# Performance work log

Hardware: AMD Instinct MI355X
Metric: run time of the kernel (lower is better)

The kernel has to match this reference:

```python
import jax, jax.numpy as jnp
import numpy as np

EMBED_DIM = 1024
NUM_HEADS = 16
HEAD_DIM = EMBED_DIM // NUM_HEADS
B, S = 2, 2048


def setup_inputs() -> dict:
    key = jax.random.key(0)
    k = jax.random.split(key, 8)
    scale = 1.0 / np.sqrt(EMBED_DIM)
    return {
        "x": jax.random.normal(k[0], (B, S, EMBED_DIM), dtype=jnp.float32),
        "x1": jax.random.normal(k[1], (B, S, EMBED_DIM), dtype=jnp.float32),
        "x2": jax.random.normal(k[2], (B, S, EMBED_DIM), dtype=jnp.float32),
        "qkv_w": jax.random.normal(k[3], (3 * EMBED_DIM, EMBED_DIM), dtype=jnp.float32) * scale,
        "qkv_b": jnp.zeros((3 * EMBED_DIM,), dtype=jnp.float32),
        "out_w": jax.random.normal(k[4], (EMBED_DIM, EMBED_DIM), dtype=jnp.float32) * scale,
        "out_b": jnp.zeros((EMBED_DIM,), dtype=jnp.float32),
    }


def reference(x, x1, x2, qkv_w, qkv_b, out_w, out_b):
    # x1, x2 are accepted but unused, matching the torch module.
    b, s, e = x.shape
    qkv = x @ qkv_w.T + qkv_b                      # [B,S,3E]
    qkv = qkv.reshape(b, s, 3, NUM_HEADS, HEAD_DIM)
    qkv = jnp.transpose(qkv, (2, 0, 3, 1, 4))      # [3,B,H,S,D]
    q, k, v = qkv[0], qkv[1], qkv[2]
    scores = jnp.einsum("bhqd,bhkd->bhqk", q, k) / np.sqrt(HEAD_DIM)
    probs = jax.nn.sigmoid(scores)                 # [B,H,S,S]
    sample = jax.random.bernoulli(jax.random.key(42), probs).astype(probs.dtype)
    # straight-through: forward uses sample, gradient flows as identity to probs
    attn = probs + jax.lax.stop_gradient(sample - probs)
    out = jnp.einsum("bhqk,bhkd->bhqd", attn, v)   # [B,H,S,D]
    out = jnp.transpose(out, (0, 2, 1, 3)).reshape(b, s, e)
    return out @ out_w.T + out_b
```

## Files before the change

### kernel.cpp

```cpp
#include <hip/hip_runtime.h>
#include <stdint.h>

#define NB 2
#define NS 2048
#define NE 1024
#define NH 16
#define ND 64

typedef __attribute__((ext_vector_type(8))) short short8;
typedef __attribute__((ext_vector_type(4))) float f4;
typedef __attribute__((ext_vector_type(4))) unsigned short us4;

static __device__ __forceinline__ unsigned short bf16_rne(float x) {
  uint32_t u = __builtin_bit_cast(uint32_t, x);
  u += 0x7fffu + ((u >> 16) & 1u);
  return (unsigned short)(u >> 16);
}
static __device__ __forceinline__ float bf16_f32(unsigned short h) {
  uint32_t u = ((uint32_t)h) << 16;
  return __builtin_bit_cast(float, u);
}

static __device__ __forceinline__ void threefry42(uint32_t x0, uint32_t x1,
                                                  uint32_t& o0, uint32_t& o1) {
  const uint32_t ks0 = 0u, ks1 = 42u;
  const uint32_t ks2 = 0u ^ 42u ^ 0x1BD11BDAu;
  x0 += ks0; x1 += ks1;
#define TF4(a,b,c,d) \
  x0 += x1; x1 = __builtin_rotateleft32(x1, a); x1 ^= x0; \
  x0 += x1; x1 = __builtin_rotateleft32(x1, b); x1 ^= x0; \
  x0 += x1; x1 = __builtin_rotateleft32(x1, c); x1 ^= x0; \
  x0 += x1; x1 = __builtin_rotateleft32(x1, d); x1 ^= x0;
  TF4(13,15,26,6)  x0 += ks1; x1 += ks2 + 1u;
  TF4(17,29,16,24) x0 += ks2; x1 += ks0 + 2u;
  TF4(13,15,26,6)  x0 += ks0; x1 += ks1 + 3u;
  TF4(17,29,16,24) x0 += ks1; x1 += ks2 + 4u;
  TF4(13,15,26,6)  x0 += ks2; x1 += ks0 + 5u;
#undef TF4
  o0 = x0; o1 = x1;
}

static __device__ __forceinline__ void gl2lds16(const void* g, void* l) {
  __builtin_amdgcn_global_load_lds(
      (const __attribute__((address_space(1))) uint32_t*)g,
      (__attribute__((address_space(3))) uint32_t*)l, 16, 0, 0);
}

__global__ void k_split(const float* __restrict__ x, const float* __restrict__ qw,
                        const float* __restrict__ ow,
                        unsigned short* __restrict__ xh, unsigned short* __restrict__ xl,
                        unsigned short* __restrict__ wh, unsigned short* __restrict__ wl,
                        unsigned short* __restrict__ woh) {
  for (uint32_t i = blockIdx.x * 256u + threadIdx.x; i < 8388608u; i += gridDim.x * 256u) {
    if (i < 4194304u) {
      float v = x[i];
      unsigned short hi = bf16_rne(v);
      xh[i] = hi;
      xl[i] = bf16_rne(v - bf16_f32(hi));
    } else if (i < 7340032u) {
      uint32_t j = i - 4194304u;
      float v = qw[j];
      unsigned short hi = bf16_rne(v);
      wh[j] = hi;
      wl[j] = bf16_rne(v - bf16_f32(hi));
    } else {
      uint32_t j = i - 7340032u;
      woh[j] = bf16_rne(ow[j]);
    }
  }
}

__global__ __launch_bounds__(256) void k_qkv(
    const unsigned short* __restrict__ xh, const unsigned short* __restrict__ xl,
    const unsigned short* __restrict__ wh, const unsigned short* __restrict__ wl,
    const float* __restrict__ qkv_b,
    unsigned short* __restrict__ Qh, unsigned short* __restrict__ Ql,
    unsigned short* __restrict__ Kh, unsigned short* __restrict__ Kl,
    unsigned short* __restrict__ Vt) {
  __shared__ unsigned short SM[16384];
  unsigned short* Ah = SM;
  unsigned short* Al = SM + 4096;
  unsigned short* Bh = SM + 8192;
  unsigned short* Bl = SM + 12288;
  const int tid = threadIdx.x;
  const int lane = tid & 63, wid = tid >> 6;
  const int wm = wid >> 1, wn = wid & 1;
  const int bn = blockIdx.x, bm = blockIdx.y;
  const bool isV = (bn >= 16);
  const int quad = lane >> 4, c16 = lane & 15;
  const int ldrow = lane >> 2;
  const int ldk = (lane & 3) * 8;

  f4 acc[4][4];
#pragma unroll
  for (int a = 0; a < 4; ++a)
#pragma unroll
    for (int b = 0; b < 4; ++b) { f4 z = {0.f, 0.f, 0.f, 0.f}; acc[a][b] = z; }

  for (int kt = 0; kt < 32; ++kt) {
    const int k0 = kt * 32;
    __syncthreads();
#pragma unroll
    for (int r = 0; r < 2; ++r) {
      const int c = wid + r * 4;
      const int grow = c * 16 + ldrow;
      const size_t ao = (size_t)(bm * 128 + grow) * 1024 + k0 + ldk;
      const size_t bo = (size_t)(bn * 128 + grow) * 1024 + k0 + ldk;
      const int lo = c * 512 + lane * 8;
      gl2lds16(xh + ao, &Ah[lo]);
      gl2lds16(wh + bo, &Bh[lo]);
      if (!isV) {
        gl2lds16(xl + ao, &Al[lo]);
        gl2lds16(wl + bo, &Bl[lo]);
      }
    }
    __syncthreads();

    short8 ah[4], al[4], bhf[4], blf[4];
#pragma unroll
    for (int t = 0; t < 4; ++t) {
      ah[t] = *(const short8*)&Ah[(wm * 64 + t * 16 + c16) * 32 + quad * 8];
      bhf[t] = *(const short8*)&Bh[(wn * 64 + t * 16 + c16) * 32 + quad * 8];
      if (!isV) {
        al[t] = *(const short8*)&Al[(wm * 64 + t * 16 + c16) * 32 + quad * 8];
        blf[t] = *(const short8*)&Bl[(wn * 64 + t * 16 + c16) * 32 + quad * 8];
      }
    }
    if (isV) {
#pragma unroll
      for (int tm = 0; tm < 4; ++tm)
#pragma unroll
        for (int tn = 0; tn < 4; ++tn)
          acc[tm][tn] = __builtin_amdgcn_mfma_f32_16x16x32_bf16(ah[tm], bhf[tn], acc[tm][tn], 0, 0, 0);
    } else {
#pragma unroll
      for (int tm = 0; tm < 4; ++tm)
#pragma unroll
        for (int tn = 0; tn < 4; ++tn) {
          acc[tm][tn] = __builtin_amdgcn_mfma_f32_16x16x32_bf16(ah[tm], bhf[tn], acc[tm][tn], 0, 0, 0);
          acc[tm][tn] = __builtin_amdgcn_mfma_f32_16x16x32_bf16(ah[tm], blf[tn], acc[tm][tn], 0, 0, 0);
          acc[tm][tn] = __builtin_amdgcn_mfma_f32_16x16x32_bf16(al[tm], bhf[tn], acc[tm][tn], 0, 0, 0);
        }
    }
  }

  if (!isV) {
#pragma unroll
    for (int tm = 0; tm < 4; ++tm) {
#pragma unroll
      for (int tn = 0; tn < 4; ++tn) {
        const int j = bn * 128 + wn * 64 + tn * 16 + c16;
        const float bias = qkv_b[j];
        const int which = j >> 10;
        const int rem = j & 1023;
        const int h = rem >> 6, d = rem & 63;
#pragma unroll
        for (int r = 0; r < 4; ++r) {
          const int i = bm * 128 + wm * 64 + tm * 16 + quad * 4 + r;
          const int b = i >> 11, s = i & 2047;
          const size_t off = (((size_t)(b * 16 + h)) * 2048 + (size_t)s) * 64 + d;
          const float v = acc[tm][tn][r] + bias;
          const unsigned short hi = bf16_rne(v);
          const unsigned short lo = bf16_rne(v - bf16_f32(hi));
          if (which == 0) { Qh[off] = hi; Ql[off] = lo; }
          else            { Kh[off] = hi; Kl[off] = lo; }
        }
      }
    }
  } else {
    __syncthreads();
#pragma unroll
    for (int tm = 0; tm < 4; ++tm) {
#pragma unroll
      for (int tn = 0; tn < 4; ++tn) {
        const int j = bn * 128 + wn * 64 + tn * 16 + c16;
        const float bias = qkv_b[j];
        const int d_local = wn * 64 + tn * 16 + c16;
#pragma unroll
        for (int r = 0; r < 4; ++r) {
          const int s_local = wm * 64 + tm * 16 + quad * 4 + r;
          SM[d_local * 128 + s_local] = bf16_rne(acc[tm][tn][r] + bias);
        }
      }
    }
    __syncthreads();
    const int b = (bm * 128) >> 11;
    const int s0 = (bm * 128) & 2047;
    const int h2 = (bn - 16) * 2;
#pragma unroll
    for (int it = 0; it < 8; ++it) {
      const int chunk = it * 256 + tid;
      const int dr = chunk >> 4;
      const int sc = (chunk & 15) * 8;
      const short8 v = *(const short8*)&SM[dr * 128 + sc];
      const int bh = b * 16 + h2 + (dr >> 6);
      const int d = dr & 63;
      *(short8*)&Vt[((size_t)bh * 64 + d) * 2048 + s0 + sc] = v;
    }
  }
}

__global__ __launch_bounds__(512, 8) void k_attn(
    const unsigned short* __restrict__ Qh, const unsigned short* __restrict__ Ql,
    const unsigned short* __restrict__ Khg, const unsigned short* __restrict__ Klg,
    const unsigned short* __restrict__ Vtg, unsigned short* __restrict__ AO) {
  __shared__ unsigned short Ksh[4096], Ksl[4096], Vs[8192];
  __shared__ unsigned char Pmb[8192];
  const int tid = threadIdx.x;
  const int lane = tid & 63, w = tid >> 6;
  const int quad = lane >> 4, c16 = lane & 15;
  const int q0 = blockIdx.x * 128;
  const int bh = blockIdx.y;
  const int ks = blockIdx.z;
  const int kbase = ks * 1024;
  const size_t base = (size_t)bh * (size_t)(2048 * 64);
  unsigned short* AOp = AO + (size_t)ks * 4194304u;

  const size_t qoff = base + (size_t)(q0 + w * 16 + c16) * 64 + quad * 8;
  const short8 qh0 = *(const short8*)&Qh[qoff];
  const short8 qh1 = *(const short8*)&Qh[qoff + 32];
  const short8 ql0 = *(const short8*)&Ql[qoff];
  const short8 ql1 = *(const short8*)&Ql[qoff + 32];

  const uint32_t fb = (uint32_t)bh * 4194304u +
                      (uint32_t)(q0 + w * 16 + quad * 4) * 2048u + (uint32_t)c16;

  const int r0 = tid >> 3, g0 = ((tid & 7) - r0) & 7;

  f4 oacc[4];
#pragma unroll
  for (int s = 0; s < 4; ++s) { f4 z = {0.f, 0.f, 0.f, 0.f}; oacc[s] = z; }

  auto stage = [&](int kb, int vbuf) {
    const size_t koff = base + (size_t)kb * 64;
    gl2lds16(Khg + koff + r0 * 64 + g0 * 8, &Ksh[tid * 8]);
    gl2lds16(Klg + koff + r0 * 64 + g0 * 8, &Ksl[tid * 8]);
    gl2lds16(Vtg + base + (size_t)r0 * 2048 + kb + g0 * 8, &Vs[vbuf * 4096 + tid * 8]);
  };

  stage(kbase, 0);

  for (int kt = 0; kt < 16; ++kt) {
    const int kb = kbase + kt * 64;
    const int vb = (kt & 1) * 4096;
    __syncthreads();

    f4 sacc[4];
#pragma unroll
    for (int sub = 0; sub < 4; ++sub) {
      const int rK = sub * 16 + c16;
      const int sA = ((quad + rK) & 7) * 8;
      const int sB = ((quad + 4 + rK) & 7) * 8;
      const short8 kh0 = *(const short8*)&Ksh[rK * 64 + sA];
      const short8 kh1 = *(const short8*)&Ksh[rK * 64 + sB];
      const short8 kl0 = *(const short8*)&Ksl[rK * 64 + sA];
      const short8 kl1 = *(const short8*)&Ksl[rK * 64 + sB];
      f4 s = {0.f, 0.f, 0.f, 0.f};
      s = __builtin_amdgcn_mfma_f32_16x16x32_bf16(qh0, kh0, s, 0, 0, 0);
      s = __builtin_amdgcn_mfma_f32_16x16x32_bf16(qh1, kh1, s, 0, 0, 0);
      s = __builtin_amdgcn_mfma_f32_16x16x32_bf16(qh0, kl0, s, 0, 0, 0);
      s = __builtin_amdgcn_mfma_f32_16x16x32_bf16(qh1, kl1, s, 0, 0, 0);
      s = __builtin_amdgcn_mfma_f32_16x16x32_bf16(ql0, kh0, s, 0, 0, 0);
      s = __builtin_amdgcn_mfma_f32_16x16x32_bf16(ql1, kh1, s, 0, 0, 0);
      sacc[sub] = s;
    }
    __syncthreads();
    if (kt < 15) stage(kb + 64, (kt & 1) ^ 1);

#pragma unroll
    for (int sub = 0; sub < 4; ++sub) {
#pragma unroll
      for (int rr = 0; rr < 4; ++rr) {
        const uint32_t f = fb + (uint32_t)(rr * 2048) + (uint32_t)(kb + sub * 16);
        uint32_t o0, o1;
        threefry42(0u, f, o0, o1);
        const float m = (float)((o0 ^ o1) >> 9);
        const float e = __builtin_amdgcn_exp2f(sacc[sub][rr] * -0.18033688f);
        const int row = w * 16 + quad * 4 + rr;
        Pmb[row * 64 + sub * 16 + c16] = (fmaf(m, e, m) < 8388608.0f) ? 0x40u : 0u;
      }
    }

    const int rp = w * 16 + c16;
    const uint32_t plo0 = *(const uint32_t*)&Pmb[rp * 64 + quad * 8];
    const uint32_t phi0 = *(const uint32_t*)&Pmb[rp * 64 + quad * 8 + 4];
    const uint32_t plo1 = *(const uint32_t*)&Pmb[rp * 64 + 32 + quad * 8];
    const uint32_t phi1 = *(const uint32_t*)&Pmb[rp * 64 + 32 + quad * 8 + 4];
    short8 pa0, pa1;
#pragma unroll
    for (int j = 0; j < 4; ++j) {
      pa0[j]     = (plo0 & (0x40u << (8 * j))) ? (short)0x3F80 : (short)0;
      pa0[j + 4] = (phi0 & (0x40u << (8 * j))) ? (short)0x3F80 : (short)0;
      pa1[j]     = (plo1 & (0x40u << (8 * j))) ? (short)0x3F80 : (short)0;
      pa1[j + 4] = (phi1 & (0x40u << (8 * j))) ? (short)0x3F80 : (short)0;
    }
#pragma unroll
    for (int sub = 0; sub < 4; ++sub) {
      const int rV = sub * 16 + c16;
      const short8 vv0 = *(const short8*)&Vs[vb + rV * 64 + ((quad + rV) & 7) * 8];
      const short8 vv1 = *(const short8*)&Vs[vb + rV * 64 + ((quad + 4 + rV) & 7) * 8];
      oacc[sub] = __builtin_amdgcn_mfma_f32_16x16x32_bf16(pa0, vv0, oacc[sub], 0, 0, 0);
      oacc[sub] = __builtin_amdgcn_mfma_f32_16x16x32_bf16(pa1, vv1, oacc[sub], 0, 0, 0);
    }
  }

  const int b = bh >> 4, hh = bh & 15;
#pragma unroll
  for (int sub = 0; sub < 4; ++sub)
#pragma unroll
    for (int r = 0; r < 4; ++r) {
      const int srow = b * 2048 + q0 + w * 16 + quad * 4 + r;
      AOp[(size_t)srow * 1024 + hh * 64 + sub * 16 + c16] = bf16_rne(oacc[sub][r]);
    }
}

__global__ __launch_bounds__(256) void k_out(
    const unsigned short* __restrict__ A0, const unsigned short* __restrict__ A1,
    const unsigned short* __restrict__ Bw,
    const float* __restrict__ out_b, float* __restrict__ out) {
  __shared__ unsigned short As[128 * 32], Bs[128 * 32];
  const int tid = threadIdx.x;
  const int lane = tid & 63, wid = tid >> 6;
  const int wm = wid >> 1, wn = wid & 1;
  const int bn = blockIdx.x, bm = blockIdx.y;
  const int quad = lane >> 4, c16 = lane & 15;
  const int ldrow = lane >> 2;
  const int ldk = (lane & 3) * 8;

  f4 acc[4][4];
#pragma unroll
  for (int a = 0; a < 4; ++a)
#pragma unroll
    for (int b = 0; b < 4; ++b) { f4 z = {0.f, 0.f, 0.f, 0.f}; acc[a][b] = z; }

  for (int kt = 0; kt < 32; ++kt) {
    const int k0 = kt * 32;
    __syncthreads();
#pragma unroll
    for (int r = 0; r < 2; ++r) {
      const int c = wid + r * 4;
      const int grow = c * 16 + ldrow;
      const size_t ao = (size_t)(bm * 128 + grow) * 1024 + k0 + ldk;
      const size_t bo = (size_t)(bn * 128 + grow) * 1024 + k0 + ldk;
      const int lo = c * 512 + lane * 8;
      const short8 a0 = *(const short8*)&A0[ao];
      const short8 a1 = *(const short8*)&A1[ao];
      short8 acm;
#pragma unroll
      for (int j = 0; j < 8; ++j)
        acm[j] = (short)bf16_rne(bf16_f32((unsigned short)a0[j]) +
                                 bf16_f32((unsigned short)a1[j]));
      *(short8*)&As[lo] = acm;
      gl2lds16(Bw + bo, &Bs[lo]);
    }
    __syncthreads();

    short8 af[4], bf[4];
#pragma unroll
    for (int t = 0; t < 4; ++t) {
      af[t] = *(const short8*)&As[(wm * 64 + t * 16 + c16) * 32 + quad * 8];
      bf[t] = *(const short8*)&Bs[(wn * 64 + t * 16 + c16) * 32 + quad * 8];
    }
#pragma unroll
    for (int tm = 0; tm < 4; ++tm)
#pragma unroll
      for (int tn = 0; tn < 4; ++tn)
        acc[tm][tn] = __builtin_amdgcn_mfma_f32_16x16x32_bf16(af[tm], bf[tn], acc[tm][tn], 0, 0, 0);
  }

#pragma unroll
  for (int tm = 0; tm < 4; ++tm) {
#pragma unroll
    for (int tn = 0; tn < 4; ++tn) {
      const int j = bn * 128 + wn * 64 + tn * 16 + c16;
      const float bias = out_b[j];
#pragma unroll
      for (int r = 0; r < 4; ++r) {
        const int i = bm * 128 + wm * 64 + tm * 16 + quad * 4 + r;
        out[(size_t)i * 1024 + j] = acc[tm][tn][r] + bias;
      }
    }
  }
}

extern "C" void kernel_launch(void* const* d_in, const int* in_sizes, int n_in,
                              void* d_out, int out_size, void* d_ws, size_t ws_size,
                              hipStream_t stream) {
  const float* x     = (const float*)d_in[0];
  const float* qkv_w = (const float*)d_in[3];
  const float* qkv_b = (const float*)d_in[4];
  const float* out_w = (const float*)d_in[5];
  const float* out_b = (const float*)d_in[6];
  float* out = (float*)d_out;

  unsigned short* xh  = (unsigned short*)d_ws;
  unsigned short* xl  = xh + 4194304;
  unsigned short* wh  = xl + 4194304;
  unsigned short* wl  = wh + 3145728;
  unsigned short* woh = wl + 3145728;
  unsigned short* Vt  = woh + 1048576;
  unsigned short* Qh  = Vt + 4194304;
  unsigned short* Ql  = Qh + 4194304;
  unsigned short* Kh  = Ql + 4194304;
  unsigned short* Kl  = Kh + 4194304;
  unsigned short* AO0 = xh;
  unsigned short* AO1 = xl;

  k_split<<<8192, 256, 0, stream>>>(x, qkv_w, out_w, xh, xl, wh, wl, woh);
  k_qkv<<<dim3(24, 32), 256, 0, stream>>>(xh, xl, wh, wl, qkv_b, Qh, Ql, Kh, Kl, Vt);
  k_attn<<<dim3(16, 32, 2), 512, 0, stream>>>(Qh, Ql, Kh, Kl, Vt, AO0);
  k_out<<<dim3(8, 32), 256, 0, stream>>>(AO0, AO1, woh, out_b, out);
}
```

Baseline: 562.1 us.

## Shrink attention blocks to 64 queries and transpose masks via ds_bpermute

The attention kernel now uses 256-thread blocks covering 64 query rows, with twice as many blocks, and each thread stages two chunks of K/V per tile. The shared-memory byte mask used to transpose the Bernoulli sample from MFMA output layout to A-operand layout is replaced by per-lane bitmasks exchanged through ds_bpermute. This removes the LDS mask buffer and its writes and reads. In exchange, each K/V tile is loaded from global memory twice as often in total, and the lane shuffles add instructions.

```diff
diff --git a/kernel.cpp b/kernel.cpp
--- a/kernel.cpp
+++ b/kernel.cpp
@@ -200,16 +200,15 @@
   }
 }
 
-__global__ __launch_bounds__(512, 8) void k_attn(
+__global__ __launch_bounds__(256) void k_attn(
     const unsigned short* __restrict__ Qh, const unsigned short* __restrict__ Ql,
     const unsigned short* __restrict__ Khg, const unsigned short* __restrict__ Klg,
     const unsigned short* __restrict__ Vtg, unsigned short* __restrict__ AO) {
   __shared__ unsigned short Ksh[4096], Ksl[4096], Vs[8192];
-  __shared__ unsigned char Pmb[8192];
   const int tid = threadIdx.x;
   const int lane = tid & 63, w = tid >> 6;
   const int quad = lane >> 4, c16 = lane & 15;
-  const int q0 = blockIdx.x * 128;
+  const int q0 = blockIdx.x * 64;
   const int bh = blockIdx.y;
   const int ks = blockIdx.z;
   const int kbase = ks * 1024;
@@ -225,7 +224,11 @@
   const uint32_t fb = (uint32_t)bh * 4194304u +
                       (uint32_t)(q0 + w * 16 + quad * 4) * 2048u + (uint32_t)c16;
 
-  const int r0 = tid >> 3, g0 = ((tid & 7) - r0) & 7;
+  const int c0 = tid, r0 = c0 >> 3, g0 = ((c0 & 7) - r0) & 7;
+  const int c1 = tid + 256, r1 = c1 >> 3, g1 = ((c1 & 7) - r1) & 7;
+
+  const int lsb = (((c16 >> 2) << 4) + ((quad & 1) << 3)) << 2;
+  const int bitsel = ((quad >> 1) << 2) + (c16 & 3);
 
   f4 oacc[4];
 #pragma unroll
@@ -233,9 +236,12 @@
 
   auto stage = [&](int kb, int vbuf) {
     const size_t koff = base + (size_t)kb * 64;
-    gl2lds16(Khg + koff + r0 * 64 + g0 * 8, &Ksh[tid * 8]);
-    gl2lds16(Klg + koff + r0 * 64 + g0 * 8, &Ksl[tid * 8]);
-    gl2lds16(Vtg + base + (size_t)r0 * 2048 + kb + g0 * 8, &Vs[vbuf * 4096 + tid * 8]);
+    gl2lds16(Khg + koff + r0 * 64 + g0 * 8, &Ksh[c0 * 8]);
+    gl2lds16(Klg + koff + r0 * 64 + g0 * 8, &Ksl[c0 * 8]);
+    gl2lds16(Vtg + base + (size_t)r0 * 2048 + kb + g0 * 8, &Vs[vbuf * 4096 + c0 * 8]);
+    gl2lds16(Khg + koff + r1 * 64 + g1 * 8, &Ksh[c1 * 8]);
+    gl2lds16(Klg + koff + r1 * 64 + g1 * 8, &Ksl[c1 * 8]);
+    gl2lds16(Vtg + base + (size_t)r1 * 2048 + kb + g1 * 8, &Vs[vbuf * 4096 + c1 * 8]);
   };
 
   stage(kbase, 0);
@@ -267,6 +273,7 @@
     __syncthreads();
     if (kt < 15) stage(kb + 64, (kt & 1) ^ 1);
 
+    uint32_t pk = 0u;
 #pragma unroll
     for (int sub = 0; sub < 4; ++sub) {
 #pragma unroll
@@ -276,23 +283,17 @@
         threefry42(0u, f, o0, o1);
         const float m = (float)((o0 ^ o1) >> 9);
         const float e = __builtin_amdgcn_exp2f(sacc[sub][rr] * -0.18033688f);
-        const int row = w * 16 + quad * 4 + rr;
-        Pmb[row * 64 + sub * 16 + c16] = (fmaf(m, e, m) < 8388608.0f) ? 0x40u : 0u;
-      }
-    }
-
-    const int rp = w * 16 + c16;
-    const uint32_t plo0 = *(const uint32_t*)&Pmb[rp * 64 + quad * 8];
-    const uint32_t phi0 = *(const uint32_t*)&Pmb[rp * 64 + quad * 8 + 4];
-    const uint32_t plo1 = *(const uint32_t*)&Pmb[rp * 64 + 32 + quad * 8];
-    const uint32_t phi1 = *(const uint32_t*)&Pmb[rp * 64 + 32 + quad * 8 + 4];
+        if (fmaf(m, e, m) < 8388608.0f) pk |= (1u << (sub * 4 + rr));
+      }
+    }
+
     short8 pa0, pa1;
 #pragma unroll
-    for (int j = 0; j < 4; ++j) {
-      pa0[j]     = (plo0 & (0x40u << (8 * j))) ? (short)0x3F80 : (short)0;
-      pa0[j + 4] = (phi0 & (0x40u << (8 * j))) ? (short)0x3F80 : (short)0;
-      pa1[j]     = (plo1 & (0x40u << (8 * j))) ? (short)0x3F80 : (short)0;
-      pa1[j + 4] = (phi1 & (0x40u << (8 * j))) ? (short)0x3F80 : (short)0;
+    for (int j = 0; j < 8; ++j) {
+      const uint32_t t =
+          ((uint32_t)__builtin_amdgcn_ds_bpermute(lsb + j * 4, (int)pk)) >> bitsel;
+      pa0[j] = (t & 1u) ? (short)0x3F80 : (short)0;
+      pa1[j] = (t & 256u) ? (short)0x3F80 : (short)0;
     }
 #pragma unroll
     for (int sub = 0; sub < 4; ++sub) {
@@ -408,6 +409,6 @@
 
   k_split<<<8192, 256, 0, stream>>>(x, qkv_w, out_w, xh, xl, wh, wl, woh);
   k_qkv<<<dim3(24, 32), 256, 0, stream>>>(xh, xl, wh, wl, qkv_b, Qh, Ql, Kh, Kl, Vt);
-  k_attn<<<dim3(16, 32, 2), 512, 0, stream>>>(Qh, Ql, Kh, Kl, Vt, AO0);
+  k_attn<<<dim3(32, 32, 2), 256, 0, stream>>>(Qh, Ql, Kh, Kl, Vt, AO0);
   k_out<<<dim3(8, 32), 256, 0, stream>>>(AO0, AO1, woh, out_b, out);
 }
```

New measurement: 539.6 us. 4.0% less time.
